# Optimization experiments

Hardware: AMD Instinct MI355X
Metric: run time of the kernel (lower is better)

## Reference

```python
import jax, jax.numpy as jnp
import numpy as np

B, S, E, H, D = 4, 2048, 512, 8, 64
NEG = 1e13  # module uses -1e13, not -inf


def setup_inputs() -> dict:
    key = jax.random.key(0)
    ks = jax.random.split(key, 10)
    x = jax.random.normal(ks[0], (B, S, E), dtype=jnp.float32)
    padding_pos = jax.random.randint(ks[1], (B, S), 0, 2, dtype=jnp.int64)
    std = 0.01
    # weights stored [in, out]; torch Linear init: normal(0, 0.01) weights, default bias
    Wq = jax.random.normal(ks[2], (E, H * D), dtype=jnp.float32) * std
    Wk = jax.random.normal(ks[3], (E, H * D), dtype=jnp.float32) * std
    Wv = jax.random.normal(ks[4], (E, H * D), dtype=jnp.float32) * std
    Wo = jax.random.normal(ks[5], (H * D, E), dtype=jnp.float32) * std
    bq = jax.random.uniform(ks[6], (H * D,), dtype=jnp.float32, minval=-1, maxval=1) / np.sqrt(E)
    bk = jax.random.uniform(ks[7], (H * D,), dtype=jnp.float32, minval=-1, maxval=1) / np.sqrt(E)
    bv = jax.random.uniform(ks[8], (H * D,), dtype=jnp.float32, minval=-1, maxval=1) / np.sqrt(E)
    bo = jax.random.uniform(ks[9], (E,), dtype=jnp.float32, minval=-1, maxval=1) / np.sqrt(H * D)
    return {"x": x, "padding_pos": padding_pos, "Wq": Wq, "bq": bq, "Wk": Wk,
            "bk": bk, "Wv": Wv, "bv": bv, "Wo": Wo, "bo": bo}


def reference(x, padding_pos, Wq, bq, Wk, bk, Wv, bv, Wo, bo):
    b = x.shape[0]
    q = (x @ Wq + bq).reshape(b, S, H, D).transpose(0, 2, 1, 3)  # [B,H,S,D]
    k = (x @ Wk + bk).reshape(b, S, H, D).transpose(0, 2, 1, 3)
    v = (x @ Wv + bv).reshape(b, S, H, D).transpose(0, 2, 1, 3)
    att = jnp.einsum('bhqd,bhkd->bhqk', q, k) / jnp.sqrt(jnp.float32(D))
    pad = (padding_pos == 1)  # [B,S]
    # mask key columns and query rows (module masks both via broadcast fills)
    mask = pad[:, None, None, :] | pad[:, None, :, None]  # [B,1,S,S]
    att = jnp.where(mask, -NEG, att)
    att = jax.nn.softmax(att, axis=-1)
    out = jnp.einsum('bhqk,bhkd->bhqd', att, v)
    out = out.transpose(0, 2, 1, 3).reshape(b, S, H * D)
    return out @ Wo + bo
```

## Files before the change

### kernel.cpp

```cpp
#include <hip/hip_runtime.h>
#include <hip/hip_bf16.h>
#include <math.h>

#define Bb 4
#define Ss 2048
#define Ee 512
#define Hh 8
#define Dd 64
#define HD 512
#define Mm (Bb*Ss)

using bf16x8 = __attribute__((ext_vector_type(8))) short;
using f32x4  = __attribute__((ext_vector_type(4))) float;

typedef __attribute__((address_space(1))) const unsigned int gu32;
typedef __attribute__((address_space(3))) unsigned int lu32;
__device__ inline void glds16(const void* g, void* l) {
    __builtin_amdgcn_global_load_lds((gu32*)g, (lu32*)l, 16, 0, 0);
}

__device__ inline unsigned short f2bf(float f) {
    unsigned int u = __float_as_uint(f);
    unsigned int r = (u + 0x7fffu + ((u >> 16) & 1u)) >> 16;
    return (unsigned short)r;
}
__device__ inline float bf2f(unsigned short u) {
    return __uint_as_float((unsigned int)u << 16);
}
__device__ inline unsigned int cvtpk(float a, float b) {
    float2 t; t.x = a; t.y = b;
    union { __hip_bfloat162 h; unsigned int u; } z;
    z.h = __float22bfloat162_rn(t);
    return z.u;
}

__global__ __launch_bounds__(256) void prep(
    const float* __restrict__ x, const int* __restrict__ pad,
    const float* __restrict__ Wq, const float* __restrict__ Wk,
    const float* __restrict__ Wv, const float* __restrict__ Wo,
    unsigned short* __restrict__ Wt, unsigned short* __restrict__ xb,
    int* __restrict__ idx, int* __restrict__ cnt)
{
    __shared__ float T[64][68];
    const int bi = blockIdx.x, tid = threadIdx.x;

    if (bi < 256) {
        const int w = bi >> 6;
        const float* W = (w == 0) ? Wq : (w == 1) ? Wk : (w == 2) ? Wv : Wo;
        const int tk0 = ((bi >> 3) & 7) * 64, tn0 = (bi & 7) * 64;
        #pragma unroll
        for (int l = 0; l < 4; ++l) {
            int fi = tid + l * 256;
            int r = fi >> 4, c4 = (fi & 15) * 4;
            *(float4*)&T[r][c4] = *(const float4*)(W + (size_t)(tk0 + r) * Ee + tn0 + c4);
        }
        __syncthreads();
        #pragma unroll
        for (int l = 0; l < 4; ++l) {
            int fi = tid + l * 256;
            int r2 = fi >> 4, c4 = (fi & 15) * 4;
            uint2 o;
            o.x = cvtpk(T[c4 + 0][r2], T[c4 + 1][r2]);
            o.y = cvtpk(T[c4 + 2][r2], T[c4 + 3][r2]);
            *(uint2*)(Wt + (size_t)w * 262144 + (size_t)(tn0 + r2) * Ee + tk0 + c4) = o;
        }
    } else if (bi < 260) {
        const int b = bi - 256;
        int* sc = (int*)&T[0][0];
        int loc[8], c = 0;
        #pragma unroll
        for (int j = 0; j < 8; ++j) {
            loc[j] = pad[b * Ss + tid * 8 + j];
            c += (loc[j] == 0);
        }
        sc[tid] = c;
        __syncthreads();
        for (int s = 1; s < 256; s <<= 1) {
            int v = (tid >= s) ? sc[tid - s] : 0;
            __syncthreads();
            sc[tid] += v;
            __syncthreads();
        }
        int off = b * Ss + sc[tid] - c;
        #pragma unroll
        for (int j = 0; j < 8; ++j)
            if (loc[j] == 0) idx[off++] = tid * 8 + j;
        if (tid == 255) cnt[b] = sc[255];
    } else {
        const size_t off = (size_t)(bi - 260) * 2048 + tid * 8;
        float4 a = *(const float4*)(x + off);
        float4 bfl = *(const float4*)(x + off + 4);
        uint4 o;
        o.x = cvtpk(a.x, a.y); o.y = cvtpk(a.z, a.w);
        o.z = cvtpk(bfl.x, bfl.y); o.w = cvtpk(bfl.z, bfl.w);
        *(uint4*)(xb + off) = o;
    }
}

__global__ __launch_bounds__(256) void gemm_qkv(
    const unsigned short* __restrict__ xb, const unsigned short* __restrict__ Wt,
    const float* __restrict__ bq, const float* __restrict__ bk, const float* __restrict__ bv,
    unsigned short* __restrict__ qo, unsigned short* __restrict__ ko, unsigned short* __restrict__ vo)
{
    const int z = blockIdx.z;
    const unsigned short* Wz = Wt + (size_t)z * 262144;
    const float* bias = (z == 0) ? bq : (z == 1) ? bk : bv;
    unsigned short* dst = (z == 0) ? qo : (z == 1) ? ko : vo;

    const int m0 = blockIdx.x * 128, n0 = blockIdx.y * 128;
    const int tid = threadIdx.x, lane = tid & 63, wv = tid >> 6;
    const int quad = lane >> 4, l15 = lane & 15;
    const int wm = (wv >> 1) * 64, wn = (wv & 1) * 64;

    __shared__ unsigned short As[128][32];
    __shared__ unsigned short Bs[128][32];

    f32x4 acc[4][4] = {};

    for (int k0 = 0; k0 < Ee; k0 += 32) {
        #pragma unroll
        for (int l = 0; l < 2; ++l) {
            int ci = tid + l * 256;
            int r = ci >> 2, ch = (ci & 3) * 8;
            glds16(xb + (size_t)(m0 + r) * Ee + k0 + ch, &As[r][ch]);
            glds16(Wz + (size_t)(n0 + r) * Ee + k0 + ch, &Bs[r][ch]);
        }
        __syncthreads();

        bf16x8 af[4], bfr[4];
        #pragma unroll
        for (int ms = 0; ms < 4; ++ms) af[ms] = *(const bf16x8*)&As[wm + ms * 16 + l15][quad * 8];
        #pragma unroll
        for (int ns = 0; ns < 4; ++ns) bfr[ns] = *(const bf16x8*)&Bs[wn + ns * 16 + l15][quad * 8];
        #pragma unroll
        for (int ms = 0; ms < 4; ++ms)
            #pragma unroll
            for (int ns = 0; ns < 4; ++ns)
                acc[ms][ns] = __builtin_amdgcn_mfma_f32_16x16x32_bf16(af[ms], bfr[ns], acc[ms][ns], 0, 0, 0);
        __syncthreads();
    }

    #pragma unroll
    for (int ns = 0; ns < 4; ++ns) {
        int col = n0 + wn + ns * 16 + l15;
        float bb = bias[col];
        int h = col >> 6, d = col & 63;
        #pragma unroll
        for (int ms = 0; ms < 4; ++ms) {
            #pragma unroll
            for (int r = 0; r < 4; ++r) {
                int m = m0 + wm + ms * 16 + quad * 4 + r;
                int b = m >> 11, s = m & 2047;
                float val = acc[ms][ns][r] + bb;
                if (z == 0) val *= 0.18033688f;
                dst[((size_t)(b * Hh + h) * Ss + s) * Dd + d] = f2bf(val);
            }
        }
    }
}

__global__ __launch_bounds__(256) void compact_vmean(
    const unsigned short* __restrict__ kb, const unsigned short* __restrict__ vb,
    const int* __restrict__ idx, const int* __restrict__ cnt,
    unsigned short* __restrict__ kc, unsigned short* __restrict__ vtc,
    float* __restrict__ vmean)
{
    const int bh = blockIdx.y, b = bh >> 3;
    const int bx = blockIdx.x, tid = threadIdx.x;

    if (bx == 32) {
        __shared__ float sm[32][64];
        const int chunk = tid & 7, part = tid >> 3;
        float a8[8] = {};
        const unsigned short* p = vb + (size_t)bh * Ss * Dd + chunk * 8;
        for (int i = 0; i < 64; ++i) {
            union { unsigned short u[8]; uint4 q; } t;
            t.q = *(const uint4*)(p + (size_t)(part * 64 + i) * Dd);
            #pragma unroll
            for (int j = 0; j < 8; ++j) a8[j] += bf2f(t.u[j]);
        }
        #pragma unroll
        for (int j = 0; j < 8; ++j) sm[part][chunk * 8 + j] = a8[j];
        __syncthreads();
        if (tid < 64) {
            float s = 0.f;
            #pragma unroll 8
            for (int pp = 0; pp < 32; ++pp) s += sm[pp][tid];
            vmean[bh * Dd + tid] = s * (1.0f / 2048.0f);
        }
        return;
    }

    const int cntb = cnt[b];
    const int j0 = bx * 64;
    if (j0 >= cntb) return;
    const unsigned short* kbb = kb + (size_t)bh * Ss * Dd;
    const unsigned short* vbb = vb + (size_t)bh * Ss * Dd;
    __shared__ unsigned short T[64][72];
    __shared__ int sidx[64];
    if (tid < 64) {
        int j = j0 + tid;
        sidx[tid] = (j < cntb) ? idx[b * Ss + j] : -1;
    }
    __syncthreads();
    #pragma unroll
    for (int l = 0; l < 2; ++l) {
        int ci = tid + l * 256;
        int r = ci >> 3, ch = (ci & 7) * 8;
        int s = sidx[r];
        uint4 kd = {0, 0, 0, 0}, vd = {0, 0, 0, 0};
        if (s >= 0) {
            kd = *(const uint4*)(kbb + (size_t)s * Dd + ch);
            vd = *(const uint4*)(vbb + (size_t)s * Dd + ch);
        }
        *(uint4*)(kc + ((size_t)bh * Ss + j0 + r) * Dd + ch) = kd;
        *(uint4*)&T[r][ch] = vd;
    }
    __syncthreads();
    #pragma unroll
    for (int l = 0; l < 2; ++l) {
        int ci = tid + l * 256;
        int dr = ci >> 3, sc8 = (ci & 7) * 8;
        union { unsigned short u[8]; uint4 q; } o;
        #pragma unroll
        for (int j = 0; j < 8; ++j) o.u[j] = T[sc8 + j][dr];
        *(uint4*)(vtc + ((size_t)bh * Dd + dr) * Ss + j0 + sc8) = o.q;
    }
}

__global__ __launch_bounds__(256) void attn(
    const unsigned short* __restrict__ q, const unsigned short* __restrict__ kc,
    const unsigned short* __restrict__ vtc, const int* __restrict__ pad,
    const int* __restrict__ cnt, const float* __restrict__ vmean,
    unsigned short* __restrict__ ao)
{
    __shared__ unsigned short Ks[2][64][32];
    __shared__ unsigned short Vs[2][64][32];
    __shared__ float Ps[4][16][68];

    const int tid = threadIdx.x, wv = tid >> 6, lane = tid & 63;
    const int quad = lane >> 4, l15 = lane & 15;
    const int bh = blockIdx.y, b = bh >> 3, h = bh & 7;
    const int q0 = blockIdx.x * 128 + wv * 32;

    const unsigned short* qb  = q   + (size_t)bh * Ss * Dd;
    const unsigned short* kcb = kc  + (size_t)bh * Ss * Dd;
    const unsigned short* vtb = vtc + (size_t)bh * Dd * Ss;

    const int cntb = cnt[b];
    const int ktiles = (cntb + 63) >> 6;
    const bool tail = (cntb & 63) != 0;

    bf16x8 aq[2][2];
    #pragma unroll
    for (int g = 0; g < 2; ++g) {
        aq[g][0] = *(const bf16x8*)(qb + (size_t)(q0 + g * 16 + l15) * Dd + quad * 8);
        aq[g][1] = *(const bf16x8*)(qb + (size_t)(q0 + g * 16 + l15) * Dd + 32 + quad * 8);
    }

    bool qp[2][4];
    #pragma unroll
    for (int g = 0; g < 2; ++g)
        #pragma unroll
        for (int r = 0; r < 4; ++r)
            qp[g][r] = pad[b * Ss + q0 + g * 16 + quad * 4 + r] != 0;

    float li[2][4] = {};
    f32x4 oacc[2][4] = {};

    for (int kt = 0; kt < ktiles; ++kt) {
        const int k0 = kt * 64;
        __syncthreads();
        #pragma unroll
        for (int l = 0; l < 2; ++l) {
            int ci = tid + l * 256;
            int s = ci >> 8, row = (ci >> 2) & 63, ch = (ci & 3) * 8;
            glds16(kcb + (size_t)(k0 + row) * Dd + s * 32 + ch, &Ks[s][row][ch]);
            glds16(vtb + (size_t)row * Ss + k0 + s * 32 + ch, &Vs[s][row][ch]);
        }
        __syncthreads();

        bf16x8 kf[4][2], vf[4][2];
        #pragma unroll
        for (int nt = 0; nt < 4; ++nt) {
            kf[nt][0] = *(const bf16x8*)&Ks[0][nt * 16 + l15][quad * 8];
            kf[nt][1] = *(const bf16x8*)&Ks[1][nt * 16 + l15][quad * 8];
            vf[nt][0] = *(const bf16x8*)&Vs[0][nt * 16 + l15][quad * 8];
            vf[nt][1] = *(const bf16x8*)&Vs[1][nt * 16 + l15][quad * 8];
        }

        #pragma unroll
        for (int g = 0; g < 2; ++g) {
            f32x4 sa[4];
            #pragma unroll
            for (int nt = 0; nt < 4; ++nt) {
                f32x4 zz = {0.f, 0.f, 0.f, 0.f};
                zz = __builtin_amdgcn_mfma_f32_16x16x32_bf16(aq[g][0], kf[nt][0], zz, 0, 0, 0);
                zz = __builtin_amdgcn_mfma_f32_16x16x32_bf16(aq[g][1], kf[nt][1], zz, 0, 0, 0);
                sa[nt] = zz;
            }

            if (tail && kt == ktiles - 1) {
                #pragma unroll
                for (int nt = 0; nt < 4; ++nt) {
                    bool bad = (k0 + nt * 16 + l15) >= cntb;
                    #pragma unroll
                    for (int r = 0; r < 4; ++r)
                        if (bad) sa[nt][r] = -1e30f;
                }
            }

            #pragma unroll
            for (int nt = 0; nt < 4; ++nt)
                #pragma unroll
                for (int r = 0; r < 4; ++r) {
                    float p = exp2f(sa[nt][r]);
                    sa[nt][r] = p;
                    li[g][r] += p;
                }

            #pragma unroll
            for (int r = 0; r < 4; ++r) {
                int qrow = quad * 4 + r;
                #pragma unroll
                for (int nt = 0; nt < 4; ++nt)
                    Ps[wv][qrow][nt * 16 + l15] = sa[nt][r];
            }
            float4 p0 = *(const float4*)&Ps[wv][l15][quad * 8];
            float4 p1 = *(const float4*)&Ps[wv][l15][quad * 8 + 4];
            float4 p2 = *(const float4*)&Ps[wv][l15][32 + quad * 8];
            float4 p3 = *(const float4*)&Ps[wv][l15][32 + quad * 8 + 4];
            union U8 { unsigned int u[4]; bf16x8 v8; };
            U8 ap0, ap1;
            ap0.u[0] = cvtpk(p0.x, p0.y); ap0.u[1] = cvtpk(p0.z, p0.w);
            ap0.u[2] = cvtpk(p1.x, p1.y); ap0.u[3] = cvtpk(p1.z, p1.w);
            ap1.u[0] = cvtpk(p2.x, p2.y); ap1.u[1] = cvtpk(p2.z, p2.w);
            ap1.u[2] = cvtpk(p3.x, p3.y); ap1.u[3] = cvtpk(p3.z, p3.w);

            #pragma unroll
            for (int nt = 0; nt < 4; ++nt) {
                oacc[g][nt] = __builtin_amdgcn_mfma_f32_16x16x32_bf16(ap0.v8, vf[nt][0], oacc[g][nt], 0, 0, 0);
                oacc[g][nt] = __builtin_amdgcn_mfma_f32_16x16x32_bf16(ap1.v8, vf[nt][1], oacc[g][nt], 0, 0, 0);
            }
        }
    }

    #pragma unroll
    for (int g = 0; g < 2; ++g) {
        #pragma unroll
        for (int r = 0; r < 4; ++r) {
            float ls = li[g][r];
            ls += __shfl_xor(ls, 1);
            ls += __shfl_xor(ls, 2);
            ls += __shfl_xor(ls, 4);
            ls += __shfl_xor(ls, 8);
            float inv = (ls > 0.f) ? 1.0f / ls : 0.f;
            int srow = q0 + g * 16 + quad * 4 + r;
            #pragma unroll
            for (int nt = 0; nt < 4; ++nt) {
                int d = nt * 16 + l15;
                float val = qp[g][r] ? vmean[bh * Dd + d] : oacc[g][nt][r] * inv;
                ao[((size_t)b * Ss + srow) * HD + h * Dd + d] = f2bf(val);
            }
        }
    }
}

__global__ __launch_bounds__(256) void gemm_out(
    const unsigned short* __restrict__ a_in, const unsigned short* __restrict__ Wt,
    const float* __restrict__ bo, float* __restrict__ out)
{
    const unsigned short* Wz = Wt + (size_t)3 * 262144;
    const int m0 = blockIdx.x * 128, n0 = blockIdx.y * 128;
    const int tid = threadIdx.x, lane = tid & 63, wv = tid >> 6;
    const int quad = lane >> 4, l15 = lane & 15;
    const int wm = (wv >> 1) * 64, wn = (wv & 1) * 64;

    __shared__ unsigned short As[128][32];
    __shared__ unsigned short Bs[128][32];

    f32x4 acc[4][4] = {};

    for (int k0 = 0; k0 < HD; k0 += 32) {
        #pragma unroll
        for (int l = 0; l < 2; ++l) {
            int ci = tid + l * 256;
            int r = ci >> 2, ch = (ci & 3) * 8;
            glds16(a_in + (size_t)(m0 + r) * HD + k0 + ch, &As[r][ch]);
            glds16(Wz + (size_t)(n0 + r) * HD + k0 + ch, &Bs[r][ch]);
        }
        __syncthreads();
        bf16x8 af[4], bfr[4];
        #pragma unroll
        for (int ms = 0; ms < 4; ++ms) af[ms] = *(const bf16x8*)&As[wm + ms * 16 + l15][quad * 8];
        #pragma unroll
        for (int ns = 0; ns < 4; ++ns) bfr[ns] = *(const bf16x8*)&Bs[wn + ns * 16 + l15][quad * 8];
        #pragma unroll
        for (int ms = 0; ms < 4; ++ms)
            #pragma unroll
            for (int ns = 0; ns < 4; ++ns)
                acc[ms][ns] = __builtin_amdgcn_mfma_f32_16x16x32_bf16(af[ms], bfr[ns], acc[ms][ns], 0, 0, 0);
        __syncthreads();
    }

    #pragma unroll
    for (int ns = 0; ns < 4; ++ns) {
        int col = n0 + wn + ns * 16 + l15;
        float bb = bo[col];
        #pragma unroll
        for (int ms = 0; ms < 4; ++ms) {
            #pragma unroll
            for (int r = 0; r < 4; ++r) {
                int m = m0 + wm + ms * 16 + quad * 4 + r;
                out[(size_t)m * Ee + col] = acc[ms][ns][r] + bb;
            }
        }
    }
}

extern "C" void kernel_launch(void* const* d_in, const int* in_sizes, int n_in,
                              void* d_out, int out_size, void* d_ws, size_t ws_size,
                              hipStream_t stream) {
    const float* x   = (const float*)d_in[0];
    const int*   pad = (const int*)  d_in[1];
    const float* Wq  = (const float*)d_in[2];
    const float* bq  = (const float*)d_in[3];
    const float* Wk  = (const float*)d_in[4];
    const float* bk  = (const float*)d_in[5];
    const float* Wv  = (const float*)d_in[6];
    const float* bv  = (const float*)d_in[7];
    const float* Wo  = (const float*)d_in[8];
    const float* bo  = (const float*)d_in[9];
    float* out = (float*)d_out;

    const size_t tsz = (size_t)Bb * Hh * Ss * Dd;
    unsigned short* Wt  = (unsigned short*)d_ws;
    unsigned short* qb  = Wt + 1048576;
    unsigned short* kb  = qb + tsz;
    unsigned short* vb  = kb + tsz;
    unsigned short* kc  = vb + tsz;
    unsigned short* xb  = kc + tsz;
    unsigned short* vtc = xb;
    unsigned short* aob = kb;
    int* idxw   = (int*)(xb + tsz);
    int* cntw   = idxw + Bb * Ss;
    float* vmw  = (float*)(cntw + 4);

    prep<<<2308, 256, 0, stream>>>(x, pad, Wq, Wk, Wv, Wo, Wt, xb, idxw, cntw);

    dim3 g1(Mm / 128, HD / 128, 3);
    gemm_qkv<<<g1, 256, 0, stream>>>(xb, Wt, bq, bk, bv, qb, kb, vb);

    dim3 g2(33, Bb * Hh);
    compact_vmean<<<g2, 256, 0, stream>>>(kb, vb, idxw, cntw, kc, vtc, vmw);

    dim3 g3(Ss / 128, Bb * Hh);
    attn<<<g3, 256, 0, stream>>>(qb, kc, vtc, pad, cntw, vmw, aob);

    dim3 g4(Mm / 128, Ee / 128);
    gemm_out<<<g4, 256, 0, stream>>>(aob, Wt, bo, out);
}
```

Measured before the change: 185.1 us.

## Double-buffer LDS tiles in GEMMs and attention, store QKV row-major

```diff
diff --git a/kernel.cpp b/kernel.cpp
--- a/kernel.cpp
+++ b/kernel.cpp
@@ -112,48 +112,55 @@
     const int quad = lane >> 4, l15 = lane & 15;
     const int wm = (wv >> 1) * 64, wn = (wv & 1) * 64;
 
-    __shared__ unsigned short As[128][32];
-    __shared__ unsigned short Bs[128][32];
+    __shared__ unsigned short As0[128][32], Bs0[128][32];
+    __shared__ unsigned short As1[128][32], Bs1[128][32];
 
     f32x4 acc[4][4] = {};
 
-    for (int k0 = 0; k0 < Ee; k0 += 32) {
+    auto stage = [&](unsigned short (&A)[128][32], unsigned short (&B)[128][32], int k0) {
         #pragma unroll
         for (int l = 0; l < 2; ++l) {
             int ci = tid + l * 256;
             int r = ci >> 2, ch = (ci & 3) * 8;
-            glds16(xb + (size_t)(m0 + r) * Ee + k0 + ch, &As[r][ch]);
-            glds16(Wz + (size_t)(n0 + r) * Ee + k0 + ch, &Bs[r][ch]);
-        }
-        __syncthreads();
-
+            glds16(xb + (size_t)(m0 + r) * Ee + k0 + ch, &A[r][ch]);
+            glds16(Wz + (size_t)(n0 + r) * Ee + k0 + ch, &B[r][ch]);
+        }
+    };
+    auto compute = [&](const unsigned short (&A)[128][32], const unsigned short (&B)[128][32]) {
         bf16x8 af[4], bfr[4];
         #pragma unroll
-        for (int ms = 0; ms < 4; ++ms) af[ms] = *(const bf16x8*)&As[wm + ms * 16 + l15][quad * 8];
-        #pragma unroll
-        for (int ns = 0; ns < 4; ++ns) bfr[ns] = *(const bf16x8*)&Bs[wn + ns * 16 + l15][quad * 8];
+        for (int ms = 0; ms < 4; ++ms) af[ms] = *(const bf16x8*)&A[wm + ms * 16 + l15][quad * 8];
+        #pragma unroll
+        for (int ns = 0; ns < 4; ++ns) bfr[ns] = *(const bf16x8*)&B[wn + ns * 16 + l15][quad * 8];
         #pragma unroll
         for (int ms = 0; ms < 4; ++ms)
             #pragma unroll
             for (int ns = 0; ns < 4; ++ns)
                 acc[ms][ns] = __builtin_amdgcn_mfma_f32_16x16x32_bf16(af[ms], bfr[ns], acc[ms][ns], 0, 0, 0);
-        __syncthreads();
+    };
+
+    stage(As0, Bs0, 0);
+    for (int ki = 0; ki < 16; ki += 2) {
+        __syncthreads();
+        if (ki + 1 < 16) stage(As1, Bs1, (ki + 1) * 32);
+        compute(As0, Bs0);
+        __syncthreads();
+        if (ki + 2 < 16) stage(As0, Bs0, (ki + 2) * 32);
+        compute(As1, Bs1);
     }
 
     #pragma unroll
     for (int ns = 0; ns < 4; ++ns) {
         int col = n0 + wn + ns * 16 + l15;
         float bb = bias[col];
-        int h = col >> 6, d = col & 63;
         #pragma unroll
         for (int ms = 0; ms < 4; ++ms) {
             #pragma unroll
             for (int r = 0; r < 4; ++r) {
                 int m = m0 + wm + ms * 16 + quad * 4 + r;
-                int b = m >> 11, s = m & 2047;
                 float val = acc[ms][ns][r] + bb;
                 if (z == 0) val *= 0.18033688f;
-                dst[((size_t)(b * Hh + h) * Ss + s) * Dd + d] = f2bf(val);
+                dst[(size_t)m * HD + col] = f2bf(val);
             }
         }
     }
@@ -165,17 +172,17 @@
     unsigned short* __restrict__ kc, unsigned short* __restrict__ vtc,
     float* __restrict__ vmean)
 {
-    const int bh = blockIdx.y, b = bh >> 3;
+    const int bh = blockIdx.y, b = bh >> 3, h = bh & 7;
     const int bx = blockIdx.x, tid = threadIdx.x;
 
     if (bx == 32) {
         __shared__ float sm[32][64];
         const int chunk = tid & 7, part = tid >> 3;
         float a8[8] = {};
-        const unsigned short* p = vb + (size_t)bh * Ss * Dd + chunk * 8;
+        const unsigned short* p = vb + (size_t)b * Ss * HD + h * Dd + chunk * 8;
         for (int i = 0; i < 64; ++i) {
             union { unsigned short u[8]; uint4 q; } t;
-            t.q = *(const uint4*)(p + (size_t)(part * 64 + i) * Dd);
+            t.q = *(const uint4*)(p + (size_t)(part * 64 + i) * HD);
             #pragma unroll
             for (int j = 0; j < 8; ++j) a8[j] += bf2f(t.u[j]);
         }
@@ -194,8 +201,6 @@
     const int cntb = cnt[b];
     const int j0 = bx * 64;
     if (j0 >= cntb) return;
-    const unsigned short* kbb = kb + (size_t)bh * Ss * Dd;
-    const unsigned short* vbb = vb + (size_t)bh * Ss * Dd;
     __shared__ unsigned short T[64][72];
     __shared__ int sidx[64];
     if (tid < 64) {
@@ -210,8 +215,9 @@
         int s = sidx[r];
         uint4 kd = {0, 0, 0, 0}, vd = {0, 0, 0, 0};
         if (s >= 0) {
-            kd = *(const uint4*)(kbb + (size_t)s * Dd + ch);
-            vd = *(const uint4*)(vbb + (size_t)s * Dd + ch);
+            size_t row = (size_t)(b * Ss + s) * HD + h * Dd;
+            kd = *(const uint4*)(kb + row + ch);
+            vd = *(const uint4*)(vb + row + ch);
         }
         *(uint4*)(kc + ((size_t)bh * Ss + j0 + r) * Dd + ch) = kd;
         *(uint4*)&T[r][ch] = vd;
@@ -234,16 +240,15 @@
     const int* __restrict__ cnt, const float* __restrict__ vmean,
     unsigned short* __restrict__ ao)
 {
-    __shared__ unsigned short Ks[2][64][32];
-    __shared__ unsigned short Vs[2][64][32];
+    __shared__ unsigned short Ks0[2][64][32], Vs0[2][64][32];
+    __shared__ unsigned short Ks1[2][64][32], Vs1[2][64][32];
     __shared__ float Ps[4][16][68];
 
     const int tid = threadIdx.x, wv = tid >> 6, lane = tid & 63;
     const int quad = lane >> 4, l15 = lane & 15;
-    const int bh = blockIdx.y, b = bh >> 3, h = bh & 7;
-    const int q0 = blockIdx.x * 128 + wv * 32;
-
-    const unsigned short* qb  = q   + (size_t)bh * Ss * Dd;
+    const int bh = blockIdx.x, b = bh >> 3, h = bh & 7;
+    const int q0 = blockIdx.y * 128 + wv * 32;
+
     const unsigned short* kcb = kc  + (size_t)bh * Ss * Dd;
     const unsigned short* vtb = vtc + (size_t)bh * Dd * Ss;
 
@@ -254,8 +259,9 @@
     bf16x8 aq[2][2];
     #pragma unroll
     for (int g = 0; g < 2; ++g) {
-        aq[g][0] = *(const bf16x8*)(qb + (size_t)(q0 + g * 16 + l15) * Dd + quad * 8);
-        aq[g][1] = *(const bf16x8*)(qb + (size_t)(q0 + g * 16 + l15) * Dd + 32 + quad * 8);
+        size_t row = (size_t)(b * Ss + q0 + g * 16 + l15) * HD + h * Dd;
+        aq[g][0] = *(const bf16x8*)(q + row + quad * 8);
+        aq[g][1] = *(const bf16x8*)(q + row + 32 + quad * 8);
     }
 
     bool qp[2][4];
@@ -268,27 +274,27 @@
     float li[2][4] = {};
     f32x4 oacc[2][4] = {};
 
-    for (int kt = 0; kt < ktiles; ++kt) {
+    auto stage = [&](unsigned short (&K)[2][64][32], unsigned short (&V)[2][64][32], int kt) {
         const int k0 = kt * 64;
-        __syncthreads();
         #pragma unroll
         for (int l = 0; l < 2; ++l) {
             int ci = tid + l * 256;
             int s = ci >> 8, row = (ci >> 2) & 63, ch = (ci & 3) * 8;
-            glds16(kcb + (size_t)(k0 + row) * Dd + s * 32 + ch, &Ks[s][row][ch]);
-            glds16(vtb + (size_t)row * Ss + k0 + s * 32 + ch, &Vs[s][row][ch]);
-        }
-        __syncthreads();
-
+            glds16(kcb + (size_t)(k0 + row) * Dd + s * 32 + ch, &K[s][row][ch]);
+            glds16(vtb + (size_t)row * Ss + k0 + s * 32 + ch, &V[s][row][ch]);
+        }
+    };
+
+    auto compute = [&](const unsigned short (&K)[2][64][32], const unsigned short (&V)[2][64][32], int kt) {
+        const int k0 = kt * 64;
         bf16x8 kf[4][2], vf[4][2];
         #pragma unroll
         for (int nt = 0; nt < 4; ++nt) {
-            kf[nt][0] = *(const bf16x8*)&Ks[0][nt * 16 + l15][quad * 8];
-            kf[nt][1] = *(const bf16x8*)&Ks[1][nt * 16 + l15][quad * 8];
-            vf[nt][0] = *(const bf16x8*)&Vs[0][nt * 16 + l15][quad * 8];
-            vf[nt][1] = *(const bf16x8*)&Vs[1][nt * 16 + l15][quad * 8];
-        }
-
+            kf[nt][0] = *(const bf16x8*)&K[0][nt * 16 + l15][quad * 8];
+            kf[nt][1] = *(const bf16x8*)&K[1][nt * 16 + l15][quad * 8];
+            vf[nt][0] = *(const bf16x8*)&V[0][nt * 16 + l15][quad * 8];
+            vf[nt][1] = *(const bf16x8*)&V[1][nt * 16 + l15][quad * 8];
+        }
         #pragma unroll
         for (int g = 0; g < 2; ++g) {
             f32x4 sa[4];
@@ -299,7 +305,6 @@
                 zz = __builtin_amdgcn_mfma_f32_16x16x32_bf16(aq[g][1], kf[nt][1], zz, 0, 0, 0);
                 sa[nt] = zz;
             }
-
             if (tail && kt == ktiles - 1) {
                 #pragma unroll
                 for (int nt = 0; nt < 4; ++nt) {
@@ -309,7 +314,6 @@
                         if (bad) sa[nt][r] = -1e30f;
                 }
             }
-
             #pragma unroll
             for (int nt = 0; nt < 4; ++nt)
                 #pragma unroll
@@ -318,7 +322,6 @@
                     sa[nt][r] = p;
                     li[g][r] += p;
                 }
-
             #pragma unroll
             for (int r = 0; r < 4; ++r) {
                 int qrow = quad * 4 + r;
@@ -336,13 +339,25 @@
             ap0.u[2] = cvtpk(p1.x, p1.y); ap0.u[3] = cvtpk(p1.z, p1.w);
             ap1.u[0] = cvtpk(p2.x, p2.y); ap1.u[1] = cvtpk(p2.z, p2.w);
             ap1.u[2] = cvtpk(p3.x, p3.y); ap1.u[3] = cvtpk(p3.z, p3.w);
-
             #pragma unroll
             for (int nt = 0; nt < 4; ++nt) {
                 oacc[g][nt] = __builtin_amdgcn_mfma_f32_16x16x32_bf16(ap0.v8, vf[nt][0], oacc[g][nt], 0, 0, 0);
                 oacc[g][nt] = __builtin_amdgcn_mfma_f32_16x16x32_bf16(ap1.v8, vf[nt][1], oacc[g][nt], 0, 0, 0);
             }
         }
+    };
+
+    stage(Ks0, Vs0, 0);
+    int kt = 0;
+    while (true) {
+        __syncthreads();
+        if (kt + 1 < ktiles) stage(Ks1, Vs1, kt + 1);
+        compute(Ks0, Vs0, kt);
+        if (++kt >= ktiles) break;
+        __syncthreads();
+        if (kt + 1 < ktiles) stage(Ks0, Vs0, kt + 1);
+        compute(Ks1, Vs1, kt);
+        if (++kt >= ktiles) break;
     }
 
     #pragma unroll
@@ -376,31 +391,41 @@
     const int quad = lane >> 4, l15 = lane & 15;
     const int wm = (wv >> 1) * 64, wn = (wv & 1) * 64;
 
-    __shared__ unsigned short As[128][32];
-    __shared__ unsigned short Bs[128][32];
+    __shared__ unsigned short As0[128][32], Bs0[128][32];
+    __shared__ unsigned short As1[128][32], Bs1[128][32];
 
     f32x4 acc[4][4] = {};
 
-    for (int k0 = 0; k0 < HD; k0 += 32) {
+    auto stage = [&](unsigned short (&A)[128][32], unsigned short (&B)[128][32], int k0) {
         #pragma unroll
         for (int l = 0; l < 2; ++l) {
             int ci = tid + l * 256;
             int r = ci >> 2, ch = (ci & 3) * 8;
-            glds16(a_in + (size_t)(m0 + r) * HD + k0 + ch, &As[r][ch]);
-            glds16(Wz + (size_t)(n0 + r) * HD + k0 + ch, &Bs[r][ch]);
-        }
-        __syncthreads();
+            glds16(a_in + (size_t)(m0 + r) * HD + k0 + ch, &A[r][ch]);
+            glds16(Wz + (size_t)(n0 + r) * HD + k0 + ch, &B[r][ch]);
+        }
+    };
+    auto compute = [&](const unsigned short (&A)[128][32], const unsigned short (&B)[128][32]) {
         bf16x8 af[4], bfr[4];
         #pragma unroll
-        for (int ms = 0; ms < 4; ++ms) af[ms] = *(const bf16x8*)&As[wm + ms * 16 + l15][quad * 8];
-        #pragma unroll
-        for (int ns = 0; ns < 4; ++ns) bfr[ns] = *(const bf16x8*)&Bs[wn + ns * 16 + l15][quad * 8];
+        for (int ms = 0; ms < 4; ++ms) af[ms] = *(const bf16x8*)&A[wm + ms * 16 + l15][quad * 8];
+        #pragma unroll
+        for (int ns = 0; ns < 4; ++ns) bfr[ns] = *(const bf16x8*)&B[wn + ns * 16 + l15][quad * 8];
         #pragma unroll
         for (int ms = 0; ms < 4; ++ms)
             #pragma unroll
             for (int ns = 0; ns < 4; ++ns)
                 acc[ms][ns] = __builtin_amdgcn_mfma_f32_16x16x32_bf16(af[ms], bfr[ns], acc[ms][ns], 0, 0, 0);
-        __syncthreads();
+    };
+
+    stage(As0, Bs0, 0);
+    for (int ki = 0; ki < 16; ki += 2) {
+        __syncthreads();
+        if (ki + 1 < 16) stage(As1, Bs1, (ki + 1) * 32);
+        compute(As0, Bs0);
+        __syncthreads();
+        if (ki + 2 < 16) stage(As0, Bs0, (ki + 2) * 32);
+        compute(As1, Bs1);
     }
 
     #pragma unroll
@@ -454,7 +479,7 @@
     dim3 g2(33, Bb * Hh);
     compact_vmean<<<g2, 256, 0, stream>>>(kb, vb, idxw, cntw, kc, vtc, vmw);
 
-    dim3 g3(Ss / 128, Bb * Hh);
+    dim3 g3(Bb * Hh, Ss / 128);
     attn<<<g3, 256, 0, stream>>>(qb, kc, vtc, pad, cntw, vmw, aob);
 
     dim3 g4(Mm / 128, Ee / 128);
```

Result: faster. 173.0 us (-6.5%).
